# Performance work log

Hardware: AMD Instinct MI355X
Metric: run time of the kernel (lower is better)

Reference implementation:

```python
import jax, jax.numpy as jnp
import numpy as np

B, T, C = 2, 2048, 2048
H, DK, DV, K = 16, 128, 128, 4
KEY_DIM = H * DK
VALUE_DIM = H * DV
CONV_DIM = 2 * KEY_DIM + VALUE_DIM
EPS = 1e-6


def setup_inputs() -> dict:
    key = jax.random.key(0)
    ks = jax.random.split(key, 6)
    s = 0.02
    return {
        "x": jax.random.normal(ks[0], (B, T, C), jnp.float32),
        "input_pos": jnp.arange(T, dtype=jnp.int32),
        "W_qkvz": jax.random.normal(ks[1], (C, CONV_DIM + VALUE_DIM), jnp.float32) * s,
        "W_b": jax.random.normal(ks[2], (C, H), jnp.float32) * s,
        "W_a": jax.random.normal(ks[3], (C, H), jnp.float32) * s,
        "conv_w": jax.random.normal(ks[4], (CONV_DIM, 1, K), jnp.float32) * 0.3,
        "norm_w": jnp.ones((DV,), jnp.float32),
        "W_out": jax.random.normal(ks[5], (VALUE_DIM, C), jnp.float32) * s,
        "conv_state": jnp.zeros((B, CONV_DIM, K), jnp.float32),
        "recurrent_state": jnp.zeros((B, H, DK, DV), jnp.float32),
    }


def _l2norm(a):
    return a / jnp.maximum(jnp.linalg.norm(a, axis=-1, keepdims=True), 1e-12)


def reference(x, input_pos, W_qkvz, W_b, W_a, conv_w, norm_w, W_out,
              conv_state, recurrent_state):
    Bx, Tx, Cx = x.shape
    # reset state when sequence starts at position 0
    keep = 1.0 - (input_pos[0] == 0).astype(x.dtype)
    conv_state = conv_state * keep
    recurrent_state = recurrent_state * keep

    qkvz = x @ W_qkvz                                  # [B,T,conv_dim+value_dim]
    qkv, z = qkvz[..., :CONV_DIM], qkvz[..., CONV_DIM:]
    z = z.reshape(Bx, Tx, H, DV)
    beta = jax.nn.sigmoid(x @ W_b)                     # [B,T,H]
    alpha = jax.nn.sigmoid(x @ W_a)                    # [B,T,H]

    # depthwise causal conv with carried conv_state prefix
    conv_in = jnp.concatenate([conv_state, qkv.transpose(0, 2, 1)], axis=-1)  # [B,conv_dim,K+T]
    y = jax.lax.conv_general_dilated(
        conv_in, conv_w, window_strides=(1,), padding='VALID',
        dimension_numbers=('NCH', 'OIH', 'NCH'), feature_group_count=CONV_DIM)
    y = jax.nn.silu(y[:, :, -Tx:]).transpose(0, 2, 1)  # [B,T,conv_dim]

    q, k, v = jnp.split(y, [KEY_DIM, 2 * KEY_DIM], axis=-1)
    q = _l2norm(q.reshape(Bx, Tx, H, DK))
    k = _l2norm(k.reshape(Bx, Tx, H, DK))
    v = v.reshape(Bx, Tx, H, DV)

    def step(state, xs):
        q_i, k_i, v_i, a_i, b_i = xs                    # [B,H,Dk],[B,H,Dk],[B,H,Dv],[B,H],[B,H]
        new_state = (a_i[..., None, None] * state
                     + b_i[..., None, None] * (k_i[..., :, None] * v_i[..., None, :]))
        out_i = jnp.einsum('bhk,bhkv->bhv', q_i, new_state)
        return new_state, out_i

    xs = (q.transpose(1, 0, 2, 3), k.transpose(1, 0, 2, 3), v.transpose(1, 0, 2, 3),
          alpha.transpose(1, 0, 2), beta.transpose(1, 0, 2))
    _, outs = jax.lax.scan(step, recurrent_state, xs)   # outs: [T,B,H,Dv]
    output = outs.transpose(1, 0, 2, 3)                 # [B,T,H,Dv]

    # RMSNorm over head_v_dim, then gate by sigmoid(z)
    output = output * jax.lax.rsqrt(jnp.mean(output * output, axis=-1, keepdims=True) + EPS) * norm_w
    output = output * jax.nn.sigmoid(z)
    return output.reshape(Bx, Tx, -1) @ W_out
```

## Files before the change

### kernel.cpp

```cpp
#include <hip/hip_runtime.h>
#include <hip/hip_bf16.h>
#include <math.h>

#define Bb 2
#define Tt 2048
#define Cc 2048
#define Hh 16
#define CONVD 6144
#define Mrows 4096
#define NCHUNK 32

typedef __attribute__((ext_vector_type(8))) short short8v;
typedef __attribute__((ext_vector_type(4))) float floatx4;

__device__ __forceinline__ unsigned short f2bf(float f) {
    __hip_bfloat16 h = __float2bfloat16(f);
    return __builtin_bit_cast(unsigned short, h);
}

__device__ __forceinline__ void load_lds16(const void* g, void* l) {
    __builtin_amdgcn_global_load_lds(
        (const __attribute__((address_space(1))) void*)g,
        (__attribute__((address_space(3))) void*)l, 16, 0, 0);
}

__device__ __forceinline__ int swz8(int col) {
    return col ^ (((col >> 5) & 3) << 3);
}

#define LGKM0 asm volatile("s_waitcnt lgkmcnt(0)" ::: "memory")
#define VMC8  asm volatile("s_waitcnt vmcnt(8)" ::: "memory")
#define VMC4  asm volatile("s_waitcnt vmcnt(4)" ::: "memory")
#define VMC0  asm volatile("s_waitcnt vmcnt(0)" ::: "memory")
#define SCHB  __builtin_amdgcn_sched_barrier(0)
#define SBAR  __builtin_amdgcn_s_barrier()

__global__ __launch_bounds__(256) void transpose_cast2(
    const float* __restrict__ W1, unsigned short* __restrict__ WT1,
    const float* __restrict__ W2, unsigned short* __restrict__ WT2)
{
    const float* W; unsigned short* WT; int Nn;
    if (blockIdx.z == 0) { W = W1; WT = WT1; Nn = 8192; }
    else                 { W = W2; WT = WT2; Nn = 2048; if (blockIdx.x >= 64) return; }
    __shared__ float tile[32][33];
    const int n0 = blockIdx.x * 32;
    const int k0 = blockIdx.y * 32;
    const int tx = threadIdx.x & 31;
    const int ty = threadIdx.x >> 5;
#pragma unroll
    for (int r = ty; r < 32; r += 8)
        tile[r][tx] = W[(size_t)(k0 + r) * Nn + n0 + tx];
    __syncthreads();
#pragma unroll
    for (int r = ty; r < 32; r += 8)
        WT[(size_t)(n0 + r) * 2048 + k0 + tx] = f2bf(tile[tx][r]);
}

__global__ __launch_bounds__(512) void gemm256(
    const unsigned short* __restrict__ A, const unsigned short* __restrict__ Bt,
    float* __restrict__ C1, float* __restrict__ C2,
    int Kk, int lda, int ldb)
{
    __shared__ __align__(16) unsigned short A_lds[4][256 * 32];
    __shared__ __align__(16) unsigned short B_lds[4][256 * 32];

    const int tid  = threadIdx.x;
    const int wid  = tid >> 6;
    const int lane = tid & 63;
    const int wr = wid >> 2, wc = wid & 3;
    const int l15 = lane & 15, kq = lane >> 4;

    const int rr = lane >> 2;
    const int cs = (lane & 3) ^ ((rr >> 1) & 3);
    const int fch = (kq ^ ((l15 >> 1) & 3)) << 3;

    const int bid = blockIdx.y * 32 + blockIdx.x;
    const int xcd = bid & 7;
    const int idx = bid >> 3;
    const int block_m = ((xcd >> 2) * 8 + (idx >> 3)) * 256;
    const int block_n = ((xcd & 3) * 8 + (idx & 7)) * 256;

    const unsigned short* Ag = A + (size_t)block_m * lda;
    const unsigned short* Bg = Bt + (size_t)block_n * ldb;

    const int NT = Kk >> 5;

#define STG(bi, kk0) do {                                                    \
    unsigned short* la_ = &A_lds[(bi)][0];                                   \
    unsigned short* lb_ = &B_lds[(bi)][0];                                   \
    _Pragma("unroll")                                                        \
    for (int j_ = 0; j_ < 2; ++j_) {                                         \
        const int brow = wid * 32 + j_ * 16;                                 \
        load_lds16(Ag + (size_t)(brow + rr) * lda + (kk0) + cs * 8,          \
                   la_ + brow * 32);                                         \
        load_lds16(Bg + (size_t)(brow + rr) * ldb + (kk0) + cs * 8,          \
                   lb_ + brow * 32);                                         \
    }                                                                        \
} while (0)

    floatx4 acc[8][4] = {};

    STG(0, 0);
    STG(1, 32);
    STG(2, 64);
    VMC8; SCHB; SBAR;

    for (int t = 0; t < NT; ++t) {
        const unsigned short* la = &A_lds[t & 3][0];
        const unsigned short* lb = &B_lds[t & 3][0];

        short8v af[8], bf[4];
#pragma unroll
        for (int mf = 0; mf < 8; ++mf)
            af[mf] = *(const short8v*)(la + (wr * 128 + mf * 16 + l15) * 32 + fch);
#pragma unroll
        for (int nf = 0; nf < 4; ++nf)
            bf[nf] = *(const short8v*)(lb + (wc * 64 + nf * 16 + l15) * 32 + fch);

        if (t + 3 < NT) STG((t + 3) & 3, (t + 3) << 5);

        LGKM0; SCHB;
        __builtin_amdgcn_s_setprio(1);
#pragma unroll
        for (int mf = 0; mf < 8; ++mf)
#pragma unroll
            for (int nf = 0; nf < 4; ++nf)
                acc[mf][nf] = __builtin_amdgcn_mfma_f32_16x16x32_bf16(
                    af[mf], bf[nf], acc[mf][nf], 0, 0, 0);
        __builtin_amdgcn_s_setprio(0);
        SCHB;
        if (t + 1 < NT) {
            if      (t + 3 < NT) { VMC8; }
            else if (t + 2 < NT) { VMC4; }
            else                 { VMC0; }
            SCHB; SBAR;
        }
    }
#undef STG

    float* Cp; int col0; size_t ldc;
    if (block_n < 6144) { Cp = C1; col0 = block_n;        ldc = 6144; }
    else                { Cp = C2; col0 = block_n - 6144; ldc = 2048; }
#pragma unroll
    for (int mf = 0; mf < 8; ++mf)
#pragma unroll
        for (int nf = 0; nf < 4; ++nf)
#pragma unroll
            for (int r = 0; r < 4; ++r) {
                int row = block_m + wr * 128 + mf * 16 + kq * 4 + r;
                int col = col0 + wc * 64 + nf * 16 + l15;
                Cp[(size_t)row * ldc + col] = acc[mf][nf][r];
            }
}

__global__ __launch_bounds__(256) void gemm_bf16(
    const unsigned short* __restrict__ A, const unsigned short* __restrict__ Bt,
    float* __restrict__ C, int Kk, int lda, int ldb, int ldc)
{
    __shared__ __align__(16) unsigned short A_lds[128 * 64];
    __shared__ __align__(16) unsigned short B_lds[128 * 64];

    const int tid = threadIdx.x;
    const int wv = tid >> 6;
    const int lane = tid & 63;
    const int wr = wv >> 1, wc = wv & 1;
    const int l15 = lane & 15, kq = lane >> 4;
    const int rsw = (l15 & 7) << 3;

    const int nwg = gridDim.x * gridDim.y;
    const int bid = blockIdx.y * gridDim.x + blockIdx.x;
    const int wgid = (bid & 7) * (nwg >> 3) + (bid >> 3);
    const int block_m = (wgid / gridDim.x) * 128;
    const int block_n = (wgid % gridDim.x) * 128;

    const int srow = lane >> 3;
    const int scol = ((lane & 7) ^ srow) << 3;

    floatx4 acc[4][4] = {};

    for (int k0 = 0; k0 < Kk; k0 += 64) {
#pragma unroll
        for (int i = 0; i < 4; ++i) {
            const int lq = wv * 4 + i;
            const unsigned short* asrc =
                A + (size_t)(block_m + lq * 8 + srow) * lda + k0 + scol;
            load_lds16(asrc, &A_lds[lq * 512]);
            const unsigned short* bsrc =
                Bt + (size_t)(block_n + lq * 8 + srow) * ldb + k0 + scol;
            load_lds16(bsrc, &B_lds[lq * 512]);
        }
        __syncthreads();

#pragma unroll
        for (int kk = 0; kk < 2; ++kk) {
            short8v af[4], bf[4];
#pragma unroll
            for (int mf = 0; mf < 4; ++mf) {
                const int row = wr * 64 + mf * 16 + l15;
                af[mf] = *(const short8v*)&A_lds[row * 64 + ((kk * 32 + kq * 8) ^ rsw)];
            }
#pragma unroll
            for (int nf = 0; nf < 4; ++nf) {
                const int row = wc * 64 + nf * 16 + l15;
                bf[nf] = *(const short8v*)&B_lds[row * 64 + ((kk * 32 + kq * 8) ^ rsw)];
            }
#pragma unroll
            for (int mf = 0; mf < 4; ++mf)
#pragma unroll
                for (int nf = 0; nf < 4; ++nf)
                    acc[mf][nf] = __builtin_amdgcn_mfma_f32_16x16x32_bf16(
                        af[mf], bf[nf], acc[mf][nf], 0, 0, 0);
        }
        __syncthreads();
    }

#pragma unroll
    for (int mf = 0; mf < 4; ++mf)
#pragma unroll
        for (int nf = 0; nf < 4; ++nf)
#pragma unroll
            for (int r = 0; r < 4; ++r) {
                int row = block_m + wr * 64 + mf * 16 + kq * 4 + r;
                int col = block_n + wc * 64 + nf * 16 + l15;
                C[(size_t)row * ldc + col] = acc[mf][nf][r];
            }
}

__global__ __launch_bounds__(256) void ab_kernel(
    const float* __restrict__ x, const float* __restrict__ W_b,
    const float* __restrict__ W_a, float* __restrict__ beta,
    float* __restrict__ alpha, unsigned short* __restrict__ xb)
{
    const int row = blockIdx.x;
    const int tid = threadIdx.x;
    float acc[32];
#pragma unroll
    for (int u = 0; u < 32; ++u) acc[u] = 0.f;

    for (int k = tid; k < Cc; k += 256) {
        float xv = x[(size_t)row * Cc + k];
        xb[(size_t)row * Cc + k] = f2bf(xv);
        const float4* wb = (const float4*)(W_b + (size_t)k * 16);
        const float4* wa = (const float4*)(W_a + (size_t)k * 16);
#pragma unroll
        for (int u = 0; u < 4; ++u) {
            float4 b4 = wb[u];
            float4 a4 = wa[u];
            acc[u * 4 + 0] = fmaf(xv, b4.x, acc[u * 4 + 0]);
            acc[u * 4 + 1] = fmaf(xv, b4.y, acc[u * 4 + 1]);
            acc[u * 4 + 2] = fmaf(xv, b4.z, acc[u * 4 + 2]);
            acc[u * 4 + 3] = fmaf(xv, b4.w, acc[u * 4 + 3]);
            acc[16 + u * 4 + 0] = fmaf(xv, a4.x, acc[16 + u * 4 + 0]);
            acc[16 + u * 4 + 1] = fmaf(xv, a4.y, acc[16 + u * 4 + 1]);
            acc[16 + u * 4 + 2] = fmaf(xv, a4.z, acc[16 + u * 4 + 2]);
            acc[16 + u * 4 + 3] = fmaf(xv, a4.w, acc[16 + u * 4 + 3]);
        }
    }
#pragma unroll
    for (int u = 0; u < 32; ++u) {
        float v = acc[u];
        for (int off = 32; off > 0; off >>= 1) v += __shfl_down(v, off);
        acc[u] = v;
    }
    __shared__ float red[4][32];
    const int wv = tid >> 6;
    if ((tid & 63) == 0) {
#pragma unroll
        for (int u = 0; u < 32; ++u) red[wv][u] = acc[u];
    }
    __syncthreads();
    if (tid < 32) {
        float v = red[0][tid] + red[1][tid] + red[2][tid] + red[3][tid];
        float s = 1.f / (1.f + expf(-v));
        if (tid < 16) beta[(size_t)row * 16 + tid] = s;
        else          alpha[(size_t)row * 16 + (tid - 16)] = s;
    }
}

__global__ __launch_bounds__(128) void conv_kernel(
    const float* __restrict__ qkv, const float* __restrict__ conv_w,
    const float* __restrict__ conv_state, const int* __restrict__ input_pos,
    float* __restrict__ qn, float* __restrict__ kn, float* __restrict__ vv)
{
    const int tc = blockIdx.x;
    const int hs = blockIdx.y;
    const int b  = blockIdx.z;
    const int lane = threadIdx.x;
    const int kind = hs >> 4;
    const int h = hs & 15;
    const int c = kind * 2048 + h * 128 + lane;
    const int t0 = tc * 16;
    const float keep = (input_pos[0] == 0) ? 0.f : 1.f;

    const float4 w4 = *(const float4*)(conv_w + (size_t)c * 4);

    float win0, win1, win2;
    {
        float tmp[3];
#pragma unroll
        for (int j = 0; j < 3; ++j) {
            int tau = t0 - 3 + j;
            tmp[j] = (tau >= 0) ? qkv[(size_t)(b * Tt + tau) * CONVD + c]
                   : keep * conv_state[((size_t)b * CONVD + c) * 4 + (tau + 4)];
        }
        win0 = tmp[0]; win1 = tmp[1]; win2 = tmp[2];
    }

    float y[16];
    __shared__ float red[16][2];
#pragma unroll
    for (int i = 0; i < 16; ++i) {
        float xv = qkv[(size_t)(b * Tt + t0 + i) * CONVD + c];
        float a = fmaf(w4.x, win0, fmaf(w4.y, win1, fmaf(w4.z, win2, w4.w * xv)));
        float yy = a / (1.f + expf(-a));
        win0 = win1; win1 = win2; win2 = xv;
        if (kind == 2) {
            vv[(size_t)(b * Tt + t0 + i) * 2048 + h * 128 + lane] = yy;
        } else {
            float sq = yy * yy;
            for (int off = 32; off > 0; off >>= 1) sq += __shfl_down(sq, off);
            if ((lane & 63) == 0) red[i][lane >> 6] = sq;
            y[i] = yy;
        }
    }
    if (kind == 2) return;
    __syncthreads();
#pragma unroll
    for (int i = 0; i < 16; ++i) {
        float tot = red[i][0] + red[i][1];
        float inv = 1.f / fmaxf(sqrtf(tot), 1e-12f);
        float outv = y[i] * inv;
        const size_t oidx = (size_t)(b * Tt + t0 + i) * 2048 + h * 128 + lane;
        if (kind == 0) qn[oidx] = outv;
        else           kn[oidx] = outv;
    }
}

__global__ __launch_bounds__(256) void chunk_prep(
    const float* __restrict__ kn, const float* __restrict__ vv,
    const float* __restrict__ alpha, const float* __restrict__ beta,
    float* __restrict__ logc_g, float* __restrict__ Mbuf)
{
    const int c = blockIdx.x, h = blockIdx.y, b = blockIdx.z;
    const int tid = threadIdx.x;
    const size_t bh = (size_t)b * Hh + h;

    __shared__ float K_lds[32][128];
    __shared__ float V_lds[32][128];
    __shared__ float logc_lds[64];
    __shared__ float b_lds[64];
    __shared__ float wk_lds[64];

    if (tid < 64) {
        const int row = b * Tt + c * 64 + tid;
        float a = alpha[(size_t)row * 16 + h];
        float la = logf(a);
#pragma unroll
        for (int d = 1; d < 64; d <<= 1) {
            float n = __shfl_up(la, d);
            if (tid >= d) la += n;
        }
        logc_lds[tid] = la;
        logc_g[bh * Tt + c * 64 + tid] = la;
        b_lds[tid] = beta[(size_t)row * 16 + h];
    }
    __syncthreads();
    if (tid < 64) {
        wk_lds[tid] = expf(logc_lds[63] - logc_lds[tid]) * b_lds[tid];
    }
    __syncthreads();

    const int ti = tid >> 4;
    const int tj = tid & 15;
    const int tj8sw = swz8(tj * 8);
    float acc[8][8];
#pragma unroll
    for (int i = 0; i < 8; ++i)
#pragma unroll
        for (int j = 0; j < 8; ++j) acc[i][j] = 0.f;

    for (int half = 0; half < 2; ++half) {
        {
            const int sl = tid >> 3;
            const int c0 = (tid & 7) * 16;
            const int grow = b * Tt + c * 64 + half * 32 + sl;
            const float4* kp = (const float4*)(kn + (size_t)grow * 2048 + h * 128 + c0);
            const float4* vp = (const float4*)(vv + (size_t)grow * 2048 + h * 128 + c0);
#pragma unroll
            for (int u = 0; u < 4; ++u) {
                const int cl = c0 + u * 4;
                *(float4*)(&K_lds[sl][cl]) = kp[u];
                *(float4*)(&V_lds[sl][swz8(cl)]) = vp[u];
            }
        }
        __syncthreads();
#pragma unroll 4
        for (int s = 0; s < 32; ++s) {
            float w = wk_lds[half * 32 + s];
            float4 k0 = *(const float4*)(&K_lds[s][ti * 8]);
            float4 k1 = *(const float4*)(&K_lds[s][ti * 8 + 4]);
            float4 v0 = *(const float4*)(&V_lds[s][tj8sw]);
            float4 v1 = *(const float4*)(&V_lds[s][tj8sw + 4]);
            float wk[8] = {w*k0.x, w*k0.y, w*k0.z, w*k0.w, w*k1.x, w*k1.y, w*k1.z, w*k1.w};
            float vf[8] = {v0.x, v0.y, v0.z, v0.w, v1.x, v1.y, v1.z, v1.w};
#pragma unroll
            for (int i = 0; i < 8; ++i)
#pragma unroll
                for (int j = 0; j < 8; ++j)
                    acc[i][j] = fmaf(wk[i], vf[j], acc[i][j]);
        }
        __syncthreads();
    }
    float* mb = Mbuf + ((bh * NCHUNK) + c) * 16384;
#pragma unroll
    for (int i = 0; i < 8; ++i) {
        float4 o0 = {acc[i][0], acc[i][1], acc[i][2], acc[i][3]};
        float4 o1 = {acc[i][4], acc[i][5], acc[i][6], acc[i][7]};
        *(float4*)(mb + (size_t)(ti * 8 + i) * 128 + tj * 8) = o0;
        *(float4*)(mb + (size_t)(ti * 8 + i) * 128 + tj * 8 + 4) = o1;
    }
}

__global__ __launch_bounds__(256) void state_scan(
    float* __restrict__ Mbuf, const float* __restrict__ logc_g,
    const float* __restrict__ rec_state, const int* __restrict__ input_pos)
{
    const size_t g = (size_t)blockIdx.x * 256 + threadIdx.x;
    const int bh = (int)(g >> 14);
    const float keep = (input_pos[0] == 0) ? 0.f : 1.f;

    float S = keep * rec_state[g];
    const float* lc = logc_g + (size_t)bh * Tt;
    float* base = Mbuf + (size_t)(g & ~16383ull) * NCHUNK + (g & 16383);
#pragma unroll 4
    for (int c = 0; c < NCHUNK; ++c) {
        float Atot = expf(lc[c * 64 + 63]);
        float m = base[(size_t)c * 16384];
        base[(size_t)c * 16384] = S;
        S = fmaf(Atot, S, m);
    }
}

__global__ __launch_bounds__(256) void chunk_out(
    const float* __restrict__ qn, const float* __restrict__ kn,
    const float* __restrict__ vv, const float* __restrict__ beta,
    const float* __restrict__ logc_g, const float* __restrict__ Sstates,
    const float* __restrict__ norm_w, const float* __restrict__ zbuf,
    unsigned short* __restrict__ gated_b)
{
    const int c = blockIdx.x, h = blockIdx.y, b = blockIdx.z;
    const int tid = threadIdx.x;
    const int ti = tid >> 4;
    const int tj = tid & 15;
    const size_t bh = (size_t)b * Hh + h;
    const int row0 = b * Tt + c * 64;

    __shared__ float Q_lds[64][132];
    __shared__ float Bf[64 * 68];
    __shared__ float At[64][68];
    __shared__ float logc_s[64], b_s[64];

    {
        const int r = tid >> 2, c0 = (tid & 3) * 32;
        const float4* qp = (const float4*)(qn + (size_t)(row0 + r) * 2048 + h * 128 + c0);
#pragma unroll
        for (int u = 0; u < 8; ++u)
            *(float4*)(&Q_lds[r][c0 + u * 4]) = qp[u];
    }
    if (tid < 64) {
        logc_s[tid] = logc_g[bh * Tt + c * 64 + tid];
        b_s[tid] = beta[(size_t)(row0 + tid) * 16 + h];
    }

    float acc_a[4][4] = {};
    for (int kh = 0; kh < 2; ++kh) {
        __syncthreads();
        {
            const int s = tid >> 2, c0 = (tid & 3) * 16;
            const float* kp = kn + (size_t)(row0 + s) * 2048 + h * 128 + kh * 64 + c0;
#pragma unroll
            for (int u = 0; u < 16; ++u)
                Bf[(c0 + u) * 68 + s] = kp[u];
        }
        __syncthreads();
#pragma unroll 4
        for (int kk = 0; kk < 64; ++kk) {
            float a[4];
#pragma unroll
            for (int r = 0; r < 4; ++r) a[r] = Q_lds[ti * 4 + r][kh * 64 + kk];
            float4 bq = *(const float4*)(&Bf[kk * 68 + tj * 4]);
            float bb[4] = {bq.x, bq.y, bq.z, bq.w};
#pragma unroll
            for (int r = 0; r < 4; ++r)
#pragma unroll
                for (int cc = 0; cc < 4; ++cc)
                    acc_a[r][cc] = fmaf(a[r], bb[cc], acc_a[r][cc]);
        }
    }

#pragma unroll
    for (int r = 0; r < 4; ++r) {
        const int t = ti * 4 + r;
        const float lct = logc_s[t];
#pragma unroll
        for (int cc = 0; cc < 4; ++cc) {
            const int s = tj * 4 + cc;
            float w = (s <= t) ? expf(lct - logc_s[s]) * b_s[s] : 0.f;
            At[t][s] = w * acc_a[r][cc];
        }
    }

    float o[4][8] = {};
    const float* Sbase = Sstates + (bh * NCHUNK + c) * 16384;
    const int tj8sw = swz8(tj * 8);
    const int rws = tid >> 4;
    const int cl = (tid & 15) * 8;
    const int sw = swz8(cl);
    float* Sb0 = Bf;
    float* Sb1 = Bf + 2112;
    {
        __syncthreads();
        const float4* sp = (const float4*)(Sbase + (size_t)rws * 128 + cl);
        *(float4*)(&Sb0[rws * 132 + sw]) = sp[0];
        *(float4*)(&Sb0[rws * 132 + sw + 4]) = sp[1];
        __syncthreads();
    }
    for (int kb = 0; kb < 8; ++kb) {
        const float* src = (kb & 1) ? Sb1 : Sb0;
        float* dst = (kb & 1) ? Sb0 : Sb1;
        float4 nv0, nv1;
        if (kb < 7) {
            const float4* sp = (const float4*)(Sbase + (size_t)((kb + 1) * 16 + rws) * 128 + cl);
            nv0 = sp[0]; nv1 = sp[1];
        }
#pragma unroll
        for (int kk = 0; kk < 16; ++kk) {
            float a[4];
#pragma unroll
            for (int r = 0; r < 4; ++r) a[r] = Q_lds[ti * 4 + r][kb * 16 + kk];
            float4 s0 = *(const float4*)(&src[kk * 132 + tj8sw]);
            float4 s1 = *(const float4*)(&src[kk * 132 + tj8sw + 4]);
            float sv[8] = {s0.x, s0.y, s0.z, s0.w, s1.x, s1.y, s1.z, s1.w};
#pragma unroll
            for (int r = 0; r < 4; ++r)
#pragma unroll
                for (int j = 0; j < 8; ++j)
                    o[r][j] = fmaf(a[r], sv[j], o[r][j]);
        }
        if (kb < 7) {
            *(float4*)(&dst[rws * 132 + sw]) = nv0;
            *(float4*)(&dst[rws * 132 + sw + 4]) = nv1;
        }
        __syncthreads();
    }
#pragma unroll
    for (int r = 0; r < 4; ++r) {
        const float ct = expf(logc_s[ti * 4 + r]);
#pragma unroll
        for (int j = 0; j < 8; ++j) o[r][j] *= ct;
    }

    for (int sh = 0; sh < 2; ++sh) {
        __syncthreads();
        {
            const int rr = tid >> 3;
            const int c0 = (tid & 7) * 16;
            const float4* vp = (const float4*)(vv + (size_t)(row0 + sh * 32 + rr) * 2048 + h * 128 + c0);
#pragma unroll
            for (int u = 0; u < 4; ++u) {
                const int clv = c0 + u * 4;
                *(float4*)(&Bf[rr * 132 + swz8(clv)]) = vp[u];
            }
        }
        __syncthreads();
#pragma unroll 2
        for (int sp = 0; sp < 32; ++sp) {
            const int s = sh * 32 + sp;
            float a[4];
#pragma unroll
            for (int r = 0; r < 4; ++r) a[r] = At[ti * 4 + r][s];
            float4 v0 = *(const float4*)(&Bf[sp * 132 + tj8sw]);
            float4 v1 = *(const float4*)(&Bf[sp * 132 + tj8sw + 4]);
            float vf[8] = {v0.x, v0.y, v0.z, v0.w, v1.x, v1.y, v1.z, v1.w};
#pragma unroll
            for (int r = 0; r < 4; ++r)
#pragma unroll
                for (int j = 0; j < 8; ++j)
                    o[r][j] = fmaf(a[r], vf[j], o[r][j]);
        }
    }

#pragma unroll
    for (int r = 0; r < 4; ++r) {
        float ss = 0.f;
#pragma unroll
        for (int j = 0; j < 8; ++j) ss = fmaf(o[r][j], o[r][j], ss);
        ss += __shfl_xor(ss, 1);
        ss += __shfl_xor(ss, 2);
        ss += __shfl_xor(ss, 4);
        ss += __shfl_xor(ss, 8);
        const float scale = rsqrtf(ss * (1.f / 128.f) + 1e-6f);
        const int t = ti * 4 + r;
        const float* zp = zbuf + (size_t)(row0 + t) * 2048 + h * 128 + tj * 8;
        unsigned short* gp = gated_b + (size_t)(row0 + t) * 2048 + h * 128 + tj * 8;
#pragma unroll
        for (int j = 0; j < 8; ++j) {
            float zv = zp[j];
            float g = o[r][j] * scale * norm_w[tj * 8 + j] * (1.f / (1.f + expf(-zv)));
            gp[j] = f2bf(g);
        }
    }
}

extern "C" void kernel_launch(void* const* d_in, const int* in_sizes, int n_in,
                              void* d_out, int out_size, void* d_ws, size_t ws_size,
                              hipStream_t stream) {
    (void)in_sizes; (void)n_in; (void)out_size; (void)ws_size;
    const float* x          = (const float*)d_in[0];
    const int*   input_pos  = (const int*)d_in[1];
    const float* W_qkvz     = (const float*)d_in[2];
    const float* W_b        = (const float*)d_in[3];
    const float* W_a        = (const float*)d_in[4];
    const float* conv_w     = (const float*)d_in[5];
    const float* norm_w     = (const float*)d_in[6];
    const float* W_out      = (const float*)d_in[7];
    const float* conv_state = (const float*)d_in[8];
    const float* rec_state  = (const float*)d_in[9];
    float* out = (float*)d_out;
    float* ws  = (float*)d_ws;

    float* qkv   = ws;
    float* Mbuf  = ws;
    unsigned short* gated_b = (unsigned short*)(ws + 16777216);
    float* qn    = ws + 25165824ull;
    float* kn    = qn + 8388608ull;
    float* vv    = kn + 8388608ull;
    unsigned short* xb  = (unsigned short*)qn;
    unsigned short* WqT = (unsigned short*)(qn + 4194304ull);
    float* zbuf  = vv + 8388608ull;
    unsigned short* WoT = (unsigned short*)(zbuf + 8388608ull);
    float* alpha = zbuf + 8388608ull + 2097152ull;
    float* beta  = alpha + 65536ull;
    float* logc  = beta + 65536ull;

    transpose_cast2<<<dim3(256, 64, 2), 256, 0, stream>>>(W_qkvz, WqT, W_out, WoT);
    ab_kernel<<<Mrows, 256, 0, stream>>>(x, W_b, W_a, beta, alpha, xb);

    gemm256<<<dim3(8192 / 256, Mrows / 256), 512, 0, stream>>>(
        xb, WqT, qkv, zbuf, 2048, 2048, 2048);
    conv_kernel<<<dim3(Tt / 16, 48, Bb), 128, 0, stream>>>(
        qkv, conv_w, conv_state, input_pos, qn, kn, vv);
    chunk_prep<<<dim3(NCHUNK, Hh, Bb), 256, 0, stream>>>(
        kn, vv, alpha, beta, logc, Mbuf);
    state_scan<<<2048, 256, 0, stream>>>(Mbuf, logc, rec_state, input_pos);
    chunk_out<<<dim3(NCHUNK, Hh, Bb), 256, 0, stream>>>(
        qn, kn, vv, beta, logc, Mbuf, norm_w, zbuf, gated_b);
    gemm_bf16<<<dim3(2048 / 128, Mrows / 128), 256, 0, stream>>>(
        gated_b, WoT, out, 2048, 2048, 2048, 2048);
}
```

Before: 517.9 us.

## Pipeline bf16 GEMM with 4-stage LDS ring buffer and async prefetch

Restructures the generic bf16 GEMM main loop into a 4-buffer LDS ring with K-step 32, issuing global-to-LDS loads three tiles ahead and waiting on vmcnt counters instead of full barriers around each load. It also changes the LDS swizzle to match the 32-wide tiles and raises wave priority around the MFMA block. The aim is to hide global memory latency behind MFMA work, at the cost of more LDS use and fragile hand-tuned wait counts.

New measurement: 516.1 us. About the same (-0.4%).

```diff
diff --git a/kernel.cpp b/kernel.cpp
--- a/kernel.cpp
+++ b/kernel.cpp
@@ -157,15 +157,18 @@
     const unsigned short* __restrict__ A, const unsigned short* __restrict__ Bt,
     float* __restrict__ C, int Kk, int lda, int ldb, int ldc)
 {
-    __shared__ __align__(16) unsigned short A_lds[128 * 64];
-    __shared__ __align__(16) unsigned short B_lds[128 * 64];
+    __shared__ __align__(16) unsigned short A_lds[4][128 * 32];
+    __shared__ __align__(16) unsigned short B_lds[4][128 * 32];
 
     const int tid = threadIdx.x;
-    const int wv = tid >> 6;
+    const int wid = tid >> 6;
     const int lane = tid & 63;
-    const int wr = wv >> 1, wc = wv & 1;
+    const int wr = wid >> 1, wc = wid & 1;
     const int l15 = lane & 15, kq = lane >> 4;
-    const int rsw = (l15 & 7) << 3;
+
+    const int rr = lane >> 2;
+    const int cs = (lane & 3) ^ ((rr >> 1) & 3);
+    const int fch = (kq ^ ((l15 >> 1) & 3)) << 3;
 
     const int nwg = gridDim.x * gridDim.y;
     const int bid = blockIdx.y * gridDim.x + blockIdx.x;
@@ -173,46 +176,63 @@
     const int block_m = (wgid / gridDim.x) * 128;
     const int block_n = (wgid % gridDim.x) * 128;
 
-    const int srow = lane >> 3;
-    const int scol = ((lane & 7) ^ srow) << 3;
+    const unsigned short* Ag = A + (size_t)block_m * lda;
+    const unsigned short* Bg = Bt + (size_t)block_n * ldb;
+
+    const int NT = Kk >> 5;
+
+#define STG1(bi, kk0) do {                                                   \
+    unsigned short* la_ = &A_lds[(bi)][0];                                   \
+    unsigned short* lb_ = &B_lds[(bi)][0];                                   \
+    _Pragma("unroll")                                                        \
+    for (int j_ = 0; j_ < 2; ++j_) {                                         \
+        const int brow = wid * 32 + j_ * 16;                                 \
+        load_lds16(Ag + (size_t)(brow + rr) * lda + (kk0) + cs * 8,          \
+                   la_ + brow * 32);                                         \
+        load_lds16(Bg + (size_t)(brow + rr) * ldb + (kk0) + cs * 8,          \
+                   lb_ + brow * 32);                                         \
+    }                                                                        \
+} while (0)
 
     floatx4 acc[4][4] = {};
 
-    for (int k0 = 0; k0 < Kk; k0 += 64) {
-#pragma unroll
-        for (int i = 0; i < 4; ++i) {
-            const int lq = wv * 4 + i;
-            const unsigned short* asrc =
-                A + (size_t)(block_m + lq * 8 + srow) * lda + k0 + scol;
-            load_lds16(asrc, &A_lds[lq * 512]);
-            const unsigned short* bsrc =
-                Bt + (size_t)(block_n + lq * 8 + srow) * ldb + k0 + scol;
-            load_lds16(bsrc, &B_lds[lq * 512]);
-        }
-        __syncthreads();
-
-#pragma unroll
-        for (int kk = 0; kk < 2; ++kk) {
-            short8v af[4], bf[4];
-#pragma unroll
-            for (int mf = 0; mf < 4; ++mf) {
-                const int row = wr * 64 + mf * 16 + l15;
-                af[mf] = *(const short8v*)&A_lds[row * 64 + ((kk * 32 + kq * 8) ^ rsw)];
-            }
-#pragma unroll
-            for (int nf = 0; nf < 4; ++nf) {
-                const int row = wc * 64 + nf * 16 + l15;
-                bf[nf] = *(const short8v*)&B_lds[row * 64 + ((kk * 32 + kq * 8) ^ rsw)];
-            }
-#pragma unroll
-            for (int mf = 0; mf < 4; ++mf)
-#pragma unroll
-                for (int nf = 0; nf < 4; ++nf)
-                    acc[mf][nf] = __builtin_amdgcn_mfma_f32_16x16x32_bf16(
-                        af[mf], bf[nf], acc[mf][nf], 0, 0, 0);
-        }
-        __syncthreads();
-    }
+    STG1(0, 0);
+    STG1(1, 32);
+    STG1(2, 64);
+    VMC8; SCHB; SBAR;
+
+    for (int t = 0; t < NT; ++t) {
+        const unsigned short* la = &A_lds[t & 3][0];
+        const unsigned short* lb = &B_lds[t & 3][0];
+
+        short8v af[4], bf[4];
+#pragma unroll
+        for (int mf = 0; mf < 4; ++mf)
+            af[mf] = *(const short8v*)(la + (wr * 64 + mf * 16 + l15) * 32 + fch);
+#pragma unroll
+        for (int nf = 0; nf < 4; ++nf)
+            bf[nf] = *(const short8v*)(lb + (wc * 64 + nf * 16 + l15) * 32 + fch);
+
+        if (t + 3 < NT) STG1((t + 3) & 3, (t + 3) << 5);
+
+        LGKM0; SCHB;
+        __builtin_amdgcn_s_setprio(1);
+#pragma unroll
+        for (int mf = 0; mf < 4; ++mf)
+#pragma unroll
+            for (int nf = 0; nf < 4; ++nf)
+                acc[mf][nf] = __builtin_amdgcn_mfma_f32_16x16x32_bf16(
+                    af[mf], bf[nf], acc[mf][nf], 0, 0, 0);
+        __builtin_amdgcn_s_setprio(0);
+        SCHB;
+        if (t + 1 < NT) {
+            if      (t + 3 < NT) { VMC8; }
+            else if (t + 2 < NT) { VMC4; }
+            else                 { VMC0; }
+            SCHB; SBAR;
+        }
+    }
+#undef STG1
 
 #pragma unroll
     for (int mf = 0; mf < 4; ++mf)
```
